# Performance work log

Hardware: AMD Instinct MI355X
Metric: run time of the kernel (lower is better)

## Reference

```python
import jax, jax.numpy as jnp
import numpy as np

NUM_HEADS = 12
EMB = 768
D_KEY = 64
D_VALUE = 64
MASKED = True


def setup_inputs() -> dict:
    key = jax.random.key(0)
    k1, k2, k3, k4 = jax.random.split(key, 4)
    x = jax.random.normal(k1, (1, 4096, EMB), dtype=jnp.float32)
    q_proj = jax.random.normal(k2, (NUM_HEADS, EMB, D_KEY), dtype=jnp.float32)
    k_proj = jax.random.normal(k3, (NUM_HEADS, EMB, D_KEY), dtype=jnp.float32)
    v_proj = jax.random.normal(k4, (NUM_HEADS, EMB, D_VALUE), dtype=jnp.float32)
    return {"x": x, "q_proj": q_proj, "k_proj": k_proj, "v_proj": v_proj}


def reference(x, q_proj, k_proj, v_proj):
    # x: [B, S, E]; projections: [H, E, dk/dv]
    q = jnp.einsum("bse,hek->bhsk", x, q_proj)  # [B,H,S,dk]
    k = jnp.einsum("bse,hek->bhsk", x, k_proj)  # [B,H,S,dk]
    v = jnp.einsum("bse,hev->bhsv", x, v_proj)  # [B,H,S,dv]
    scale = jnp.sqrt(jnp.asarray(D_KEY, dtype=x.dtype))
    scores = jnp.einsum("bhsk,bhtk->bhst", q, k) / scale  # [B,H,S,S]
    if MASKED:
        S = x.shape[1]
        # causal mask: disallow attending to future positions (strict upper triangle)
        mask = jnp.triu(jnp.ones((S, S), dtype=bool), k=1)
        scores = jnp.where(mask, -jnp.inf, scores)
    attn = jax.nn.softmax(scores, axis=-1)
    out = jnp.einsum("bhst,bhtv->bhsv", attn, v)  # [B,H,S,dv]
    return out
```

## Files before the change

kernel.cpp:

```cpp
#include <hip/hip_runtime.h>
#include <hip/hip_bf16.h>

#define NH 12
#define SEQ 4096
#define E 768
#define DK 64

typedef float f32x4 __attribute__((ext_vector_type(4)));
typedef float f32x16 __attribute__((ext_vector_type(16)));
typedef __bf16 bf16x8 __attribute__((ext_vector_type(8)));
typedef __bf16 bf16x4 __attribute__((ext_vector_type(4)));
typedef unsigned u32x2 __attribute__((ext_vector_type(2)));
typedef unsigned u32x4 __attribute__((ext_vector_type(4)));

#define MFMA16(a, b, c) __builtin_amdgcn_mfma_f32_16x16x32_bf16((a), (b), (c), 0, 0, 0)
#define MFMA32(a, b, c) __builtin_amdgcn_mfma_f32_32x32x16_bf16((a), (b), (c), 0, 0, 0)

#define SCL 0.18033688011112042f
#define DEFER 10.8f

__device__ __forceinline__ void gload16(const void* g, void* l) {
    __builtin_amdgcn_global_load_lds(
        (const __attribute__((address_space(1))) void*)g,
        (__attribute__((address_space(3))) void*)l, 16, 0, 0);
}

__device__ __forceinline__ void block_sync() {
    __builtin_amdgcn_sched_barrier(0);
    __builtin_amdgcn_s_barrier();
    __builtin_amdgcn_sched_barrier(0);
}

__device__ __forceinline__ unsigned cvtpk(float lo, float hi) {
    unsigned r;
    asm("v_cvt_pk_bf16_f32 %0, %1, %2" : "=v"(r) : "v"(lo), "v"(hi));
    return r;
}
__device__ __forceinline__ u32x2 plswap(unsigned a, unsigned b) {
    return __builtin_amdgcn_permlane32_swap(a, b, false, false);
}
__device__ __forceinline__ float xhalf_max(float v) {
    u32x2 r = plswap(__float_as_uint(v), __float_as_uint(v));
    return fmaxf(__uint_as_float(r.x), __uint_as_float(r.y));
}
__device__ __forceinline__ float xhalf_add(float v) {
    u32x2 r = plswap(__float_as_uint(v), __float_as_uint(v));
    return __uint_as_float(r.x) + __uint_as_float(r.y);
}

__global__ __launch_bounds__(256) void xsplit_kernel(const float* __restrict__ x,
                                                     __bf16* __restrict__ xh,
                                                     __bf16* __restrict__ xl) {
    int i = blockIdx.x * blockDim.x + threadIdx.x;
    float4 v = ((const float4*)x)[i];
    bf16x4 h, l;
    float vv[4] = {v.x, v.y, v.z, v.w};
#pragma unroll
    for (int j = 0; j < 4; ++j) {
        __bf16 hh = (__bf16)vv[j];
        h[j] = hh;
        l[j] = (__bf16)(vv[j] - (float)hh);
    }
    ((bf16x4*)xh)[i] = h;
    ((bf16x4*)xl)[i] = l;
}

__global__ void wsplit_kernel(const float* __restrict__ qp,
                              const float* __restrict__ kp,
                              const float* __restrict__ vp,
                              __bf16* __restrict__ wtq_h, __bf16* __restrict__ wtq_l,
                              __bf16* __restrict__ wtk_h, __bf16* __restrict__ wtk_l,
                              __bf16* __restrict__ wtv_h) {
    int idx = blockIdx.x * blockDim.x + threadIdx.x;
    if (idx >= NH * E * DK) return;
    int h = idx / (E * DK);
    int rem = idx - h * E * DK;
    int k = rem / DK;
    int n = rem - k * DK;
    int o = h * DK * E + n * E + k;
    float q = qp[idx];
    __bf16 qh = (__bf16)q;
    wtq_h[o] = qh;
    wtq_l[o] = (__bf16)(q - (float)qh);
    float kk = kp[idx] * SCL;
    __bf16 kh = (__bf16)kk;
    wtk_h[o] = kh;
    wtk_l[o] = (__bf16)(kk - (float)kh);
    wtv_h[o] = (__bf16)vp[idx];
}

__global__ __launch_bounds__(256, 2) void proj_qk_kernel(
    const __bf16* __restrict__ xh, const __bf16* __restrict__ xl,
    const __bf16* __restrict__ wq_h_g, const __bf16* __restrict__ wq_l_g,
    const __bf16* __restrict__ wk_h_g, const __bf16* __restrict__ wk_l_g,
    __bf16* __restrict__ qh_o, __bf16* __restrict__ ql_o,
    __bf16* __restrict__ kh_o, __bf16* __restrict__ kl_o) {
    __shared__ char wlds[2][16384];

    const int wg = (blockIdx.x & 7) * 96 + (blockIdx.x >> 3);
    const int head = wg >> 6;
    const int rb = wg & 63;
    const int wave = threadIdx.x >> 6;
    const int lane = threadIdx.x & 63;
    const int lrow = lane & 15;
    const int lk8 = (lane >> 4) * 8;
    const int g4 = (lane >> 4) * 4;
    const int rowbase = rb * 64 + wave * 16;

    const char* wq_h_b = (const char*)(wq_h_g + head * DK * E);
    const char* wq_l_b = (const char*)(wq_l_g + head * DK * E);
    const char* wk_h_b = (const char*)(wk_h_g + head * DK * E);
    const char* wk_l_b = (const char*)(wk_l_g + head * DK * E);
    const char* base = (wave == 0) ? wq_h_b : (wave == 1) ? wq_l_b
                      : (wave == 2) ? wk_h_b : wk_l_b;
    const int srow = lane >> 2;
    const int scol = (lane & 3) * 16;

    auto STAGE = [&](int buf, int ks) {
#pragma unroll
        for (int r = 0; r < 4; ++r) {
            const char* src = base + (size_t)(r * 16 + srow) * (E * 2) + ks * 64 + scol;
            gload16(src, wlds[buf] + (wave * 4 + r) * 1024 + lane * 16);
        }
    };

    f32x4 accq[4], acck[4];
#pragma unroll
    for (int f = 0; f < 4; ++f) {
        accq[f] = (f32x4){0.f, 0.f, 0.f, 0.f};
        acck[f] = (f32x4){0.f, 0.f, 0.f, 0.f};
    }

    bf16x8 ah, al, ahn, aln;
    auto LOADA = [&](int ks, bf16x8& h, bf16x8& l) {
        size_t xo = (size_t)(rowbase + lrow) * E + ks * 32 + lk8;
        h = *(const bf16x8*)(xh + xo);
        l = *(const bf16x8*)(xl + xo);
    };

    LOADA(0, ah, al);
    STAGE(0, 0);
    int buf = 0;
    for (int ks = 0; ks < 24; ++ks) {
        if (ks < 23) {
            LOADA(ks + 1, ahn, aln);
            STAGE(buf ^ 1, ks + 1);
            asm volatile("s_waitcnt vmcnt(6)" ::: "memory");
        } else {
            asm volatile("s_waitcnt vmcnt(0)" ::: "memory");
        }
        block_sync();
#pragma unroll
        for (int f = 0; f < 4; ++f) {
            int bo = (f * 16 + lrow) * 64 + lk8 * 2;
            bf16x8 bqh = *(const bf16x8*)(wlds[buf] + bo);
            bf16x8 bql = *(const bf16x8*)(wlds[buf] + 4096 + bo);
            bf16x8 bkh = *(const bf16x8*)(wlds[buf] + 8192 + bo);
            bf16x8 bkl = *(const bf16x8*)(wlds[buf] + 12288 + bo);
            accq[f] = MFMA16(ah, bqh, accq[f]);
            accq[f] = MFMA16(ah, bql, accq[f]);
            accq[f] = MFMA16(al, bqh, accq[f]);
            acck[f] = MFMA16(ah, bkh, acck[f]);
            acck[f] = MFMA16(ah, bkl, acck[f]);
            acck[f] = MFMA16(al, bkh, acck[f]);
        }
        block_sync();
        if (ks < 23) {
            ah = ahn;
            al = aln;
        }
        buf ^= 1;
    }

    char* khb = (char*)kh_o + (size_t)head * SEQ * DK * 2;
    char* klb = (char*)kl_o + (size_t)head * SEQ * DK * 2;
#pragma unroll
    for (int f = 0; f < 4; ++f)
#pragma unroll
        for (int r = 0; r < 4; ++r) {
            int srow_o = rowbase + g4 + r;
            int d = f * 16 + lrow;
            size_t o = (size_t)head * SEQ * DK + (size_t)srow_o * DK + d;
            float qv = accq[f][r];
            __bf16 qhh = (__bf16)qv;
            qh_o[o] = qhh;
            ql_o[o] = (__bf16)(qv - (float)qhh);
            size_t ko = (size_t)(srow_o >> 6) * 8192 + ((srow_o >> 5) & 1) * 4096
                      + (size_t)f * 1024
                      + ((srow_o & 31) + 32 * ((lrow >> 3) & 1)) * 16 + (lrow & 7) * 2;
            float kv = acck[f][r];
            __bf16 khh = (__bf16)kv;
            *(__bf16*)(khb + ko) = khh;
            *(__bf16*)(klb + ko) = (__bf16)(kv - (float)khh);
        }
}

__global__ __launch_bounds__(256) void proj_v_kernel(
    const __bf16* __restrict__ xh, const __bf16* __restrict__ w_v,
    __bf16* __restrict__ vt_o) {
    __shared__ char wlds[2][4096];

    const int wg = (blockIdx.x & 7) * 96 + (blockIdx.x >> 3);
    const int head = wg >> 6;
    const int rb = wg & 63;
    const int wave = threadIdx.x >> 6;
    const int lane = threadIdx.x & 63;
    const int lrow = lane & 15;
    const int lk8 = (lane >> 4) * 8;
    const int g4 = (lane >> 4) * 4;
    const int rowbase = rb * 64 + wave * 16;

    const char* wv_b = (const char*)(w_v + head * DK * E);
    const int srow = lane >> 2;
    const int scol = (lane & 3) * 16;

    auto STAGE = [&](int buf, int ks) {
        const char* src = wv_b + (size_t)(wave * 16 + srow) * (E * 2) + ks * 64 + scol;
        gload16(src, wlds[buf] + wave * 1024 + lane * 16);
    };

    f32x4 acc[4];
#pragma unroll
    for (int f = 0; f < 4; ++f) acc[f] = (f32x4){0.f, 0.f, 0.f, 0.f};

    bf16x8 ah, ahn;
    auto LOADA = [&](int ks, bf16x8& h) {
        size_t xo = (size_t)(rowbase + lrow) * E + ks * 32 + lk8;
        h = *(const bf16x8*)(xh + xo);
    };

    LOADA(0, ah);
    STAGE(0, 0);
    int buf = 0;
    for (int ks = 0; ks < 24; ++ks) {
        if (ks < 23) {
            LOADA(ks + 1, ahn);
            STAGE(buf ^ 1, ks + 1);
            asm volatile("s_waitcnt vmcnt(2)" ::: "memory");
        } else {
            asm volatile("s_waitcnt vmcnt(0)" ::: "memory");
        }
        block_sync();
#pragma unroll
        for (int f = 0; f < 4; ++f) {
            int bo = (f * 16 + lrow) * 64 + lk8 * 2;
            bf16x8 bv = *(const bf16x8*)(wlds[buf] + bo);
            acc[f] = MFMA16(bv, ah, acc[f]);
        }
        block_sync();
        if (ks < 23) ah = ahn;
        buf ^= 1;
    }

    char* vb = (char*)vt_o + (size_t)head * DK * SEQ * 2;
#pragma unroll
    for (int f = 0; f < 4; ++f)
#pragma unroll
        for (int r = 0; r < 4; ++r) {
            int vd = f * 16 + g4 + r;
            int vs = rowbase + lrow;
            size_t vo = (size_t)(vs >> 6) * 8192 + ((vd >> 5) & 1) * 4096
                      + ((vs >> 4) & 3) * 1024
                      + ((vd & 31) + 32 * ((vs >> 3) & 1)) * 16 + (vs & 7) * 2;
            *(__bf16*)(vb + vo) = (__bf16)acc[f][r];
        }
}

__global__ __launch_bounds__(256, 2) void attn_kernel(
    const __bf16* __restrict__ qh, const __bf16* __restrict__ ql,
    const __bf16* __restrict__ kh, const __bf16* __restrict__ kl,
    const __bf16* __restrict__ vt,
    float* __restrict__ out) {
    __shared__ float cbuf[3][64][33];
    __shared__ float mlb[4][2][32];

    const int wg = (blockIdx.x & 7) * 192 + (blockIdx.x >> 3);
    const int head = wg >> 7;
    const int window = 127 - (wg & 127);
    const int rowbase = window * 32;
    const int wave = threadIdx.x >> 6;
    const int lane = threadIdx.x & 63;
    const int lq = lane & 31;
    const int lh = lane >> 5;

    const size_t hoff = (size_t)head * SEQ * DK;

    bf16x8 qBh[4], qBl[4];
    {
        const __bf16* qph = qh + hoff + (size_t)(rowbase + lq) * DK + lh * 8;
        const __bf16* qpl = ql + hoff + (size_t)(rowbase + lq) * DK + lh * 8;
#pragma unroll
        for (int ds = 0; ds < 4; ++ds) {
            qBh[ds] = *(const bf16x8*)(qph + ds * 16);
            qBl[ds] = *(const bf16x8*)(qpl + ds * 16);
        }
    }

    const char* kh_p = (const char*)(kh + hoff) + wave * 8192 + lane * 16;
    const char* kl_p = (const char*)(kl + hoff) + wave * 8192 + lane * 16;
    const char* vt_p = (const char*)(vt + (size_t)head * DK * SEQ) + wave * 8192 + lane * 16;

    f32x16 O0 = (f32x16)0.0f, O1 = (f32x16)0.0f;
    float m = -3.0e38f, lsum = 0.f;

    const int nt = (window >> 1) + 1;

    for (int t = wave; t < nt; t += 4) {
        const int kb = t * 64;

        f32x16 s0 = (f32x16)0.0f, s1 = (f32x16)0.0f;
#pragma unroll
        for (int ds = 0; ds < 4; ++ds) {
            bf16x8 ah0 = *(const bf16x8*)(kh_p + ds * 1024);
            bf16x8 al0 = *(const bf16x8*)(kl_p + ds * 1024);
            bf16x8 ah1 = *(const bf16x8*)(kh_p + 4096 + ds * 1024);
            bf16x8 al1 = *(const bf16x8*)(kl_p + 4096 + ds * 1024);
            s0 = MFMA32(ah0, qBh[ds], s0);
            s1 = MFMA32(ah1, qBh[ds], s1);
            s0 = MFMA32(al0, qBh[ds], s0);
            s1 = MFMA32(al1, qBh[ds], s1);
            s0 = MFMA32(ah0, qBl[ds], s0);
            s1 = MFMA32(ah1, qBl[ds], s1);
        }

        bf16x8 v00 = *(const bf16x8*)(vt_p + 0);
        bf16x8 v01 = *(const bf16x8*)(vt_p + 1024);
        bf16x8 v10 = *(const bf16x8*)(vt_p + 2048);
        bf16x8 v11 = *(const bf16x8*)(vt_p + 3072);
        bf16x8 w00 = *(const bf16x8*)(vt_p + 4096);
        bf16x8 w01 = *(const bf16x8*)(vt_p + 5120);
        bf16x8 w10 = *(const bf16x8*)(vt_p + 6144);
        bf16x8 w11 = *(const bf16x8*)(vt_p + 7168);

        if (kb + 63 > rowbase) {
            int qa = rowbase + lq;
#pragma unroll
            for (int r = 0; r < 16; ++r) {
                int kp = kb + ((r & 3) + 8 * (r >> 2) + 4 * lh);
                if (kp > qa) s0[r] = -1.0e30f;
                if (kp + 32 > qa) s1[r] = -1.0e30f;
            }
        }

        float x0 = fmaxf(s0[0], s0[1]), x1 = fmaxf(s0[2], s0[3]);
        float x2 = fmaxf(s0[4], s0[5]), x3 = fmaxf(s0[6], s0[7]);
#pragma unroll
        for (int r = 8; r < 16; r += 4) {
            x0 = fmaxf(x0, fmaxf(s0[r], s0[r + 1]));
            x1 = fmaxf(x1, fmaxf(s0[r + 2], s0[r + 3]));
        }
#pragma unroll
        for (int r = 0; r < 16; r += 4) {
            x2 = fmaxf(x2, fmaxf(s1[r], s1[r + 1]));
            x3 = fmaxf(x3, fmaxf(s1[r + 2], s1[r + 3]));
        }
        float mx = xhalf_max(fmaxf(fmaxf(x0, x1), fmaxf(x2, x3)));

        if (!__all(mx - m <= DEFER)) {
            float mn = fmaxf(m, mx);
            float al = exp2f(m - mn);
            m = mn;
            lsum *= al;
#pragma unroll
            for (int r = 0; r < 16; ++r) {
                float a = __shfl(al, (r & 3) + 8 * (r >> 2) + 4 * lh);
                O0[r] *= a;
                O1[r] *= a;
            }
        }

        s0 = s0 - m;
        s1 = s1 - m;
#pragma unroll
        for (int r = 0; r < 16; ++r) {
            s0[r] = exp2f(s0[r]);
            s1[r] = exp2f(s1[r]);
        }
        {
            f32x16 sv = s0 + s1;
            float p0 = 0.f, p1 = 0.f;
#pragma unroll
            for (int r = 0; r < 16; r += 4) {
                p0 += sv[r] + sv[r + 1];
                p1 += sv[r + 2] + sv[r + 3];
            }
            lsum += p0 + p1;
        }

        unsigned W0 = cvtpk(s0[0], s0[1]), W1 = cvtpk(s0[2], s0[3]);
        unsigned W2 = cvtpk(s0[4], s0[5]), W3 = cvtpk(s0[6], s0[7]);
        unsigned W4 = cvtpk(s0[8], s0[9]), W5 = cvtpk(s0[10], s0[11]);
        unsigned W6 = cvtpk(s0[12], s0[13]), W7 = cvtpk(s0[14], s0[15]);
        u32x2 rA = plswap(W0, W2), rB = plswap(W1, W3);
        u32x2 rC = plswap(W4, W6), rD = plswap(W5, W7);
        bf16x8 p00 = __builtin_bit_cast(bf16x8, (u32x4){rA.x, rB.x, rA.y, rB.y});
        bf16x8 p01 = __builtin_bit_cast(bf16x8, (u32x4){rC.x, rD.x, rC.y, rD.y});
        W0 = cvtpk(s1[0], s1[1]); W1 = cvtpk(s1[2], s1[3]);
        W2 = cvtpk(s1[4], s1[5]); W3 = cvtpk(s1[6], s1[7]);
        W4 = cvtpk(s1[8], s1[9]); W5 = cvtpk(s1[10], s1[11]);
        W6 = cvtpk(s1[12], s1[13]); W7 = cvtpk(s1[14], s1[15]);
        rA = plswap(W0, W2); rB = plswap(W1, W3);
        rC = plswap(W4, W6); rD = plswap(W5, W7);
        bf16x8 p10 = __builtin_bit_cast(bf16x8, (u32x4){rA.x, rB.x, rA.y, rB.y});
        bf16x8 p11 = __builtin_bit_cast(bf16x8, (u32x4){rC.x, rD.x, rC.y, rD.y});

        O0 = MFMA32(p00, v00, O0);
        O0 = MFMA32(p01, v01, O0);
        O0 = MFMA32(p10, v10, O0);
        O0 = MFMA32(p11, v11, O0);
        O1 = MFMA32(p00, w00, O1);
        O1 = MFMA32(p01, w01, O1);
        O1 = MFMA32(p10, w10, O1);
        O1 = MFMA32(p11, w11, O1);

        kh_p += 4 * 8192;
        kl_p += 4 * 8192;
        vt_p += 4 * 8192;
    }

    if (lh == 0) mlb[wave][0][lq] = m;
    __syncthreads();
    float mstar = fmaxf(fmaxf(mlb[0][0][lq], mlb[1][0][lq]),
                        fmaxf(mlb[2][0][lq], mlb[3][0][lq]));
    float sc = exp2f(m - mstar);
    float lp = xhalf_add(lsum) * sc;
#pragma unroll
    for (int r = 0; r < 16; ++r) {
        float a = __shfl(sc, (r & 3) + 8 * (r >> 2) + 4 * lh);
        O0[r] *= a;
        O1[r] *= a;
    }
    if (wave > 0) {
        if (lh == 0) mlb[wave][1][lq] = lp;
        float* cb = &cbuf[wave - 1][lane][0];
#pragma unroll
        for (int r = 0; r < 16; ++r) {
            cb[r] = O0[r];
            cb[16 + r] = O1[r];
        }
    }
    __syncthreads();
    if (wave == 0) {
        float ltot = lp + mlb[1][1][lq] + mlb[2][1][lq] + mlb[3][1][lq];
#pragma unroll
        for (int i = 0; i < 3; ++i) {
            const float* cb = &cbuf[i][lane][0];
#pragma unroll
            for (int r = 0; r < 16; ++r) {
                O0[r] += cb[r];
                O1[r] += cb[16 + r];
            }
        }
        float linv = 1.0f / ltot;
#pragma unroll
        for (int r = 0; r < 16; ++r) {
            int rr = (r & 3) + 8 * (r >> 2) + 4 * lh;
            float li = __shfl(linv, rr);
            size_t o = hoff + (size_t)(rowbase + rr) * DK + lq;
            out[o] = O0[r] * li;
            out[o + 32] = O1[r] * li;
        }
    }
}

extern "C" void kernel_launch(void* const* d_in, const int* in_sizes, int n_in,
                              void* d_out, int out_size, void* d_ws, size_t ws_size,
                              hipStream_t stream) {
    const float* x = (const float*)d_in[0];
    const float* qp = (const float*)d_in[1];
    const float* kp = (const float*)d_in[2];
    const float* vp = (const float*)d_in[3];
    float* out = (float*)d_out;

    const size_t WT_SZ = (size_t)NH * DK * E * 2;
    const size_t QKV_SZ = (size_t)NH * SEQ * DK * 2;
    const size_t X_SZ = (size_t)SEQ * E * 2;
    char* ws = (char*)d_ws;
    __bf16* wtq_h = (__bf16*)(ws + 0 * WT_SZ);
    __bf16* wtq_l = (__bf16*)(ws + 1 * WT_SZ);
    __bf16* wtk_h = (__bf16*)(ws + 2 * WT_SZ);
    __bf16* wtk_l = (__bf16*)(ws + 3 * WT_SZ);
    __bf16* wtv_h = (__bf16*)(ws + 4 * WT_SZ);
    char* p2 = ws + 5 * WT_SZ;
    __bf16* qh = (__bf16*)(p2 + 0 * QKV_SZ);
    __bf16* ql = (__bf16*)(p2 + 1 * QKV_SZ);
    __bf16* kh = (__bf16*)(p2 + 2 * QKV_SZ);
    __bf16* kl = (__bf16*)(p2 + 3 * QKV_SZ);
    __bf16* vt = (__bf16*)(p2 + 4 * QKV_SZ);
    char* p3 = p2 + 5 * QKV_SZ;
    __bf16* xh = (__bf16*)(p3 + 0 * X_SZ);
    __bf16* xl = (__bf16*)(p3 + 1 * X_SZ);

    hipLaunchKernelGGL(xsplit_kernel, dim3(SEQ * E / 4 / 256), dim3(256), 0, stream,
                       x, xh, xl);
    hipLaunchKernelGGL(wsplit_kernel, dim3((NH * E * DK + 255) / 256), dim3(256), 0, stream,
                       qp, kp, vp, wtq_h, wtq_l, wtk_h, wtk_l, wtv_h);
    hipLaunchKernelGGL(proj_qk_kernel, dim3(768), dim3(256), 0, stream,
                       xh, xl, wtq_h, wtq_l, wtk_h, wtk_l, qh, ql, kh, kl);
    hipLaunchKernelGGL(proj_v_kernel, dim3(768), dim3(256), 0, stream,
                       xh, wtv_h, vt);
    hipLaunchKernelGGL(attn_kernel, dim3(1536), dim3(256), 0, stream,
                       qh, ql, kh, kl, vt, out);
}
```

Before: 176.9 us.

## Split causal attention into balanced per-wave KV tasks with separate combine kernel

Replaces the per-window workgroup, in which four waves stride over the KV tiles and combine through LDS, with a flat task list. Each wave now owns one (head, window, split) task, and later windows get more splits (1 to 4) to even out the causal triangle's work. Each task writes its bf16 partial O plus max and sum to the workspace, which overwrites the now-dead weight-split buffers. A second kernel merges the partials with log-sum-exp weighting. This trades an extra launch and global partial traffic, plus reduced precision in the partial O, for better load balance and no in-block barriers.

```diff
diff --git a/kernel.cpp b/kernel.cpp
--- a/kernel.cpp
+++ b/kernel.cpp
@@ -18,6 +18,10 @@
 
 #define SCL 0.18033688011112042f
 #define DEFER 10.8f
+
+#define TPH 320
+#define NTASK 3840
+#define PART_SZ 4352
 
 __device__ __forceinline__ void gload16(const void* g, void* l) {
     __builtin_amdgcn_global_load_lds(
@@ -266,22 +270,29 @@
         }
 }
 
-__global__ __launch_bounds__(256, 2) void attn_kernel(
+__global__ __launch_bounds__(256, 2) void attn_part_kernel(
     const __bf16* __restrict__ qh, const __bf16* __restrict__ ql,
     const __bf16* __restrict__ kh, const __bf16* __restrict__ kl,
     const __bf16* __restrict__ vt,
-    float* __restrict__ out) {
-    __shared__ float cbuf[3][64][33];
-    __shared__ float mlb[4][2][32];
-
-    const int wg = (blockIdx.x & 7) * 192 + (blockIdx.x >> 3);
-    const int head = wg >> 7;
-    const int window = 127 - (wg & 127);
-    const int rowbase = window * 32;
+    char* __restrict__ part) {
+    const int blk = (blockIdx.x & 7) * 120 + (blockIdx.x >> 3);
     const int wave = threadIdx.x >> 6;
+    const int task = blk * 4 + wave;
     const int lane = threadIdx.x & 63;
     const int lq = lane & 31;
     const int lh = lane >> 5;
+
+    const int head = task / TPH;
+    const int t = task - head * TPH;
+    int w, split, nsp;
+    if (t < 32)       { w = t;                             split = 0;     nsp = 1; }
+    else if (t < 96)  { int u = t - 32;  w = 32 + (u >> 1); split = u & 1; nsp = 2; }
+    else if (t < 192) { int u = t - 96;  w = 64 + u / 3;    split = u % 3; nsp = 3; }
+    else              { int u = t - 192; w = 96 + (u >> 2); split = u & 3; nsp = 4; }
+    const int ktot = (w >> 1) + 1;
+    const int lo = (split * ktot) / nsp;
+    const int hi = ((split + 1) * ktot) / nsp;
+    const int rowbase = w * 32;
 
     const size_t hoff = (size_t)head * SEQ * DK;
 
@@ -296,17 +307,15 @@
         }
     }
 
-    const char* kh_p = (const char*)(kh + hoff) + wave * 8192 + lane * 16;
-    const char* kl_p = (const char*)(kl + hoff) + wave * 8192 + lane * 16;
-    const char* vt_p = (const char*)(vt + (size_t)head * DK * SEQ) + wave * 8192 + lane * 16;
+    const char* kh_p = (const char*)(kh + hoff) + (size_t)lo * 8192 + lane * 16;
+    const char* kl_p = (const char*)(kl + hoff) + (size_t)lo * 8192 + lane * 16;
+    const char* vt_p = (const char*)(vt + (size_t)head * DK * SEQ) + (size_t)lo * 8192 + lane * 16;
 
     f32x16 O0 = (f32x16)0.0f, O1 = (f32x16)0.0f;
     float m = -3.0e38f, lsum = 0.f;
 
-    const int nt = (window >> 1) + 1;
-
-    for (int t = wave; t < nt; t += 4) {
-        const int kb = t * 64;
+    for (int tt = lo; tt < hi; ++tt) {
+        const int kb = tt * 64;
 
         f32x16 s0 = (f32x16)0.0f, s1 = (f32x16)0.0f;
 #pragma unroll
@@ -413,54 +422,74 @@
         O1 = MFMA32(p10, w10, O1);
         O1 = MFMA32(p11, w11, O1);
 
-        kh_p += 4 * 8192;
-        kl_p += 4 * 8192;
-        vt_p += 4 * 8192;
-    }
-
-    if (lh == 0) mlb[wave][0][lq] = m;
-    __syncthreads();
-    float mstar = fmaxf(fmaxf(mlb[0][0][lq], mlb[1][0][lq]),
-                        fmaxf(mlb[2][0][lq], mlb[3][0][lq]));
-    float sc = exp2f(m - mstar);
-    float lp = xhalf_add(lsum) * sc;
-#pragma unroll
-    for (int r = 0; r < 16; ++r) {
-        float a = __shfl(sc, (r & 3) + 8 * (r >> 2) + 4 * lh);
-        O0[r] *= a;
-        O1[r] *= a;
-    }
-    if (wave > 0) {
-        if (lh == 0) mlb[wave][1][lq] = lp;
-        float* cb = &cbuf[wave - 1][lane][0];
-#pragma unroll
-        for (int r = 0; r < 16; ++r) {
-            cb[r] = O0[r];
-            cb[16 + r] = O1[r];
-        }
-    }
-    __syncthreads();
-    if (wave == 0) {
-        float ltot = lp + mlb[1][1][lq] + mlb[2][1][lq] + mlb[3][1][lq];
-#pragma unroll
-        for (int i = 0; i < 3; ++i) {
-            const float* cb = &cbuf[i][lane][0];
-#pragma unroll
-            for (int r = 0; r < 16; ++r) {
-                O0[r] += cb[r];
-                O1[r] += cb[16 + r];
-            }
-        }
-        float linv = 1.0f / ltot;
-#pragma unroll
-        for (int r = 0; r < 16; ++r) {
-            int rr = (r & 3) + 8 * (r >> 2) + 4 * lh;
-            float li = __shfl(linv, rr);
-            size_t o = hoff + (size_t)(rowbase + rr) * DK + lq;
-            out[o] = O0[r] * li;
-            out[o + 32] = O1[r] * li;
-        }
-    }
+        kh_p += 8192;
+        kl_p += 8192;
+        vt_p += 8192;
+    }
+
+    char* pb = part + (size_t)task * PART_SZ;
+    unsigned* ph = (unsigned*)pb;
+#pragma unroll
+    for (int r = 0; r < 16; r += 2) {
+        ph[(r >> 1) * 64 + lane] = cvtpk(O0[r], O0[r + 1]);
+        ph[512 + (r >> 1) * 64 + lane] = cvtpk(O1[r], O1[r + 1]);
+    }
+    float lf = xhalf_add(lsum);
+    float* pm = (float*)(pb + 4096);
+    if (lane < 32) {
+        pm[lq] = m;
+        pm[32 + lq] = lf;
+    }
+}
+
+__global__ __launch_bounds__(256) void attn_comb_kernel(
+    const char* __restrict__ part, float* __restrict__ out) {
+    const int W = blockIdx.x;
+    const int head = W >> 7, w = W & 127;
+    int tb, nsp;
+    if (w < 32)      { tb = w;                 nsp = 1; }
+    else if (w < 64) { tb = 32 + (w - 32) * 2; nsp = 2; }
+    else if (w < 96) { tb = 96 + (w - 64) * 3; nsp = 3; }
+    else             { tb = 192 + (w - 96) * 4; nsp = 4; }
+    tb += head * TPH;
+
+    const int tid = threadIdx.x;
+    const int row = tid >> 3;
+    const int d0 = (tid & 7) * 8;
+    const int lane0 = (d0 & 31) + 32 * ((row >> 2) & 1);
+    const int r = (row & 3) + 4 * (row >> 3);
+    const int word = (r >> 1) * 64;
+    const int hi16 = r & 1;
+    const char* p0 = part + (size_t)tb * PART_SZ;
+
+    float mv[4], lv[4];
+    float mstar = -3.0e38f;
+    for (int s = 0; s < nsp; ++s) {
+        const float* pm = (const float*)(p0 + s * PART_SZ + 4096);
+        mv[s] = pm[row];
+        lv[s] = pm[32 + row];
+        mstar = fmaxf(mstar, mv[s]);
+    }
+
+    float acc[8] = {0.f, 0.f, 0.f, 0.f, 0.f, 0.f, 0.f, 0.f};
+    float lt = 0.f;
+    for (int s = 0; s < nsp; ++s) {
+        float wgt = exp2f(mv[s] - mstar);
+        lt += wgt * lv[s];
+        const unsigned* pw = (const unsigned*)(p0 + s * PART_SZ + (d0 >> 5) * 2048);
+        u32x4 a = *(const u32x4*)(pw + word + lane0);
+        u32x4 b = *(const u32x4*)(pw + word + lane0 + 4);
+#pragma unroll
+        for (int j = 0; j < 8; ++j) {
+            unsigned u = (j < 4) ? a[j] : b[j - 4];
+            unsigned bits = hi16 ? (u & 0xffff0000u) : (u << 16);
+            acc[j] += wgt * __uint_as_float(bits);
+        }
+    }
+    float inv = 1.0f / lt;
+    size_t o = (size_t)head * SEQ * DK + (size_t)(w * 32 + row) * DK + d0;
+#pragma unroll
+    for (int j = 0; j < 8; ++j) out[o + j] = acc[j] * inv;
 }
 
 extern "C" void kernel_launch(void* const* d_in, const int* in_sizes, int n_in,
@@ -481,15 +510,16 @@
     __bf16* wtk_h = (__bf16*)(ws + 2 * WT_SZ);
     __bf16* wtk_l = (__bf16*)(ws + 3 * WT_SZ);
     __bf16* wtv_h = (__bf16*)(ws + 4 * WT_SZ);
-    char* p2 = ws + 5 * WT_SZ;
+    char* px = ws + 5 * WT_SZ;
+    __bf16* xh = (__bf16*)(px + 0 * X_SZ);
+    __bf16* xl = (__bf16*)(px + 1 * X_SZ);
+    char* p2 = px + 2 * X_SZ;
     __bf16* qh = (__bf16*)(p2 + 0 * QKV_SZ);
     __bf16* ql = (__bf16*)(p2 + 1 * QKV_SZ);
     __bf16* kh = (__bf16*)(p2 + 2 * QKV_SZ);
     __bf16* kl = (__bf16*)(p2 + 3 * QKV_SZ);
     __bf16* vt = (__bf16*)(p2 + 4 * QKV_SZ);
-    char* p3 = p2 + 5 * QKV_SZ;
-    __bf16* xh = (__bf16*)(p3 + 0 * X_SZ);
-    __bf16* xl = (__bf16*)(p3 + 1 * X_SZ);
+    char* part = ws;
 
     hipLaunchKernelGGL(xsplit_kernel, dim3(SEQ * E / 4 / 256), dim3(256), 0, stream,
                        x, xh, xl);
@@ -499,6 +529,8 @@
                        xh, xl, wtq_h, wtq_l, wtk_h, wtk_l, qh, ql, kh, kl);
     hipLaunchKernelGGL(proj_v_kernel, dim3(768), dim3(256), 0, stream,
                        xh, wtv_h, vt);
-    hipLaunchKernelGGL(attn_kernel, dim3(1536), dim3(256), 0, stream,
-                       qh, ql, kh, kl, vt, out);
-}
+    hipLaunchKernelGGL(attn_part_kernel, dim3(960), dim3(256), 0, stream,
+                       qh, ql, kh, kl, vt, part);
+    hipLaunchKernelGGL(attn_comb_kernel, dim3(1536), dim3(256), 0, stream,
+                       part, out);
+}
```

Result: slower. 187.8 us (+6.2%).

## Fuse V projection into QK projection and process two query blocks per attention workgroup

Applied to the files above, without the earlier changes.

The V projection kernel is merged into the QK projection kernel. One extra weight tile is staged per k-step and the x tile already in registers is reused, so one launch and a second pass over x are removed. The attention kernel now has each workgroup handle two adjacent 32-row query blocks (64 rows) against each K/V tile, halving K/V loads per query row and the grid size. The costs are higher register pressure and larger LDS use, possible lower occupancy, and coarser load balance across the causal triangle.

```diff
diff --git a/kernel.cpp b/kernel.cpp
--- a/kernel.cpp
+++ b/kernel.cpp
@@ -89,13 +89,15 @@
     wtv_h[o] = (__bf16)vp[idx];
 }
 
-__global__ __launch_bounds__(256, 2) void proj_qk_kernel(
+__global__ __launch_bounds__(256, 2) void proj_kernel(
     const __bf16* __restrict__ xh, const __bf16* __restrict__ xl,
     const __bf16* __restrict__ wq_h_g, const __bf16* __restrict__ wq_l_g,
     const __bf16* __restrict__ wk_h_g, const __bf16* __restrict__ wk_l_g,
+    const __bf16* __restrict__ wv_g,
     __bf16* __restrict__ qh_o, __bf16* __restrict__ ql_o,
-    __bf16* __restrict__ kh_o, __bf16* __restrict__ kl_o) {
-    __shared__ char wlds[2][16384];
+    __bf16* __restrict__ kh_o, __bf16* __restrict__ kl_o,
+    __bf16* __restrict__ vt_o) {
+    __shared__ char wlds[2][20480];
 
     const int wg = (blockIdx.x & 7) * 96 + (blockIdx.x >> 3);
     const int head = wg >> 6;
@@ -107,28 +109,28 @@
     const int g4 = (lane >> 4) * 4;
     const int rowbase = rb * 64 + wave * 16;
 
-    const char* wq_h_b = (const char*)(wq_h_g + head * DK * E);
-    const char* wq_l_b = (const char*)(wq_l_g + head * DK * E);
-    const char* wk_h_b = (const char*)(wk_h_g + head * DK * E);
-    const char* wk_l_b = (const char*)(wk_l_g + head * DK * E);
-    const char* base = (wave == 0) ? wq_h_b : (wave == 1) ? wq_l_b
-                      : (wave == 2) ? wk_h_b : wk_l_b;
+    const char* bases[5] = {
+        (const char*)(wq_h_g + head * DK * E), (const char*)(wq_l_g + head * DK * E),
+        (const char*)(wk_h_g + head * DK * E), (const char*)(wk_l_g + head * DK * E),
+        (const char*)(wv_g + head * DK * E)};
     const int srow = lane >> 2;
     const int scol = (lane & 3) * 16;
 
     auto STAGE = [&](int buf, int ks) {
 #pragma unroll
-        for (int r = 0; r < 4; ++r) {
-            const char* src = base + (size_t)(r * 16 + srow) * (E * 2) + ks * 64 + scol;
-            gload16(src, wlds[buf] + (wave * 4 + r) * 1024 + lane * 16);
+        for (int r = 0; r < 5; ++r) {
+            int q = wave * 5 + r;
+            const char* src = bases[q >> 2] + (size_t)((q & 3) * 16 + srow) * (E * 2) + ks * 64 + scol;
+            gload16(src, wlds[buf] + q * 1024 + lane * 16);
         }
     };
 
-    f32x4 accq[4], acck[4];
+    f32x4 accq[4], acck[4], accv[4];
 #pragma unroll
     for (int f = 0; f < 4; ++f) {
         accq[f] = (f32x4){0.f, 0.f, 0.f, 0.f};
         acck[f] = (f32x4){0.f, 0.f, 0.f, 0.f};
+        accv[f] = (f32x4){0.f, 0.f, 0.f, 0.f};
     }
 
     bf16x8 ah, al, ahn, aln;
@@ -145,7 +147,7 @@
         if (ks < 23) {
             LOADA(ks + 1, ahn, aln);
             STAGE(buf ^ 1, ks + 1);
-            asm volatile("s_waitcnt vmcnt(6)" ::: "memory");
+            asm volatile("s_waitcnt vmcnt(7)" ::: "memory");
         } else {
             asm volatile("s_waitcnt vmcnt(0)" ::: "memory");
         }
@@ -157,12 +159,14 @@
             bf16x8 bql = *(const bf16x8*)(wlds[buf] + 4096 + bo);
             bf16x8 bkh = *(const bf16x8*)(wlds[buf] + 8192 + bo);
             bf16x8 bkl = *(const bf16x8*)(wlds[buf] + 12288 + bo);
+            bf16x8 bv  = *(const bf16x8*)(wlds[buf] + 16384 + bo);
             accq[f] = MFMA16(ah, bqh, accq[f]);
             accq[f] = MFMA16(ah, bql, accq[f]);
             accq[f] = MFMA16(al, bqh, accq[f]);
             acck[f] = MFMA16(ah, bkh, acck[f]);
             acck[f] = MFMA16(ah, bkl, acck[f]);
             acck[f] = MFMA16(al, bkh, acck[f]);
+            accv[f] = MFMA16(bv, ah, accv[f]);
         }
         block_sync();
         if (ks < 23) {
@@ -174,6 +178,7 @@
 
     char* khb = (char*)kh_o + (size_t)head * SEQ * DK * 2;
     char* klb = (char*)kl_o + (size_t)head * SEQ * DK * 2;
+    char* vb = (char*)vt_o + (size_t)head * DK * SEQ * 2;
 #pragma unroll
     for (int f = 0; f < 4; ++f)
 #pragma unroll
@@ -192,77 +197,12 @@
             __bf16 khh = (__bf16)kv;
             *(__bf16*)(khb + ko) = khh;
             *(__bf16*)(klb + ko) = (__bf16)(kv - (float)khh);
-        }
-}
-
-__global__ __launch_bounds__(256) void proj_v_kernel(
-    const __bf16* __restrict__ xh, const __bf16* __restrict__ w_v,
-    __bf16* __restrict__ vt_o) {
-    __shared__ char wlds[2][4096];
-
-    const int wg = (blockIdx.x & 7) * 96 + (blockIdx.x >> 3);
-    const int head = wg >> 6;
-    const int rb = wg & 63;
-    const int wave = threadIdx.x >> 6;
-    const int lane = threadIdx.x & 63;
-    const int lrow = lane & 15;
-    const int lk8 = (lane >> 4) * 8;
-    const int g4 = (lane >> 4) * 4;
-    const int rowbase = rb * 64 + wave * 16;
-
-    const char* wv_b = (const char*)(w_v + head * DK * E);
-    const int srow = lane >> 2;
-    const int scol = (lane & 3) * 16;
-
-    auto STAGE = [&](int buf, int ks) {
-        const char* src = wv_b + (size_t)(wave * 16 + srow) * (E * 2) + ks * 64 + scol;
-        gload16(src, wlds[buf] + wave * 1024 + lane * 16);
-    };
-
-    f32x4 acc[4];
-#pragma unroll
-    for (int f = 0; f < 4; ++f) acc[f] = (f32x4){0.f, 0.f, 0.f, 0.f};
-
-    bf16x8 ah, ahn;
-    auto LOADA = [&](int ks, bf16x8& h) {
-        size_t xo = (size_t)(rowbase + lrow) * E + ks * 32 + lk8;
-        h = *(const bf16x8*)(xh + xo);
-    };
-
-    LOADA(0, ah);
-    STAGE(0, 0);
-    int buf = 0;
-    for (int ks = 0; ks < 24; ++ks) {
-        if (ks < 23) {
-            LOADA(ks + 1, ahn);
-            STAGE(buf ^ 1, ks + 1);
-            asm volatile("s_waitcnt vmcnt(2)" ::: "memory");
-        } else {
-            asm volatile("s_waitcnt vmcnt(0)" ::: "memory");
-        }
-        block_sync();
-#pragma unroll
-        for (int f = 0; f < 4; ++f) {
-            int bo = (f * 16 + lrow) * 64 + lk8 * 2;
-            bf16x8 bv = *(const bf16x8*)(wlds[buf] + bo);
-            acc[f] = MFMA16(bv, ah, acc[f]);
-        }
-        block_sync();
-        if (ks < 23) ah = ahn;
-        buf ^= 1;
-    }
-
-    char* vb = (char*)vt_o + (size_t)head * DK * SEQ * 2;
-#pragma unroll
-    for (int f = 0; f < 4; ++f)
-#pragma unroll
-        for (int r = 0; r < 4; ++r) {
             int vd = f * 16 + g4 + r;
             int vs = rowbase + lrow;
             size_t vo = (size_t)(vs >> 6) * 8192 + ((vd >> 5) & 1) * 4096
                       + ((vs >> 4) & 3) * 1024
                       + ((vd & 31) + 32 * ((vs >> 3) & 1)) * 16 + (vs & 7) * 2;
-            *(__bf16*)(vb + vo) = (__bf16)acc[f][r];
+            *(__bf16*)(vb + vo) = (__bf16)accv[f][r];
         }
 }
 
@@ -271,13 +211,15 @@
     const __bf16* __restrict__ kh, const __bf16* __restrict__ kl,
     const __bf16* __restrict__ vt,
     float* __restrict__ out) {
-    __shared__ float cbuf[3][64][33];
-    __shared__ float mlb[4][2][32];
-
-    const int wg = (blockIdx.x & 7) * 192 + (blockIdx.x >> 3);
-    const int head = wg >> 7;
-    const int window = 127 - (wg & 127);
-    const int rowbase = window * 32;
+    __shared__ float cbuf[2][3][64][33];
+    __shared__ float mlb[4][2][2][32];
+
+    const int wg = (blockIdx.x & 7) * 96 + (blockIdx.x >> 3);
+    const int head = wg >> 6;
+    const int pr = 63 - (wg & 63);
+    const int rowb0 = pr * 64;
+    const int rowb1 = pr * 64 + 32;
+    const int nt = pr + 1;
     const int wave = threadIdx.x >> 6;
     const int lane = threadIdx.x & 63;
     const int lq = lane & 31;
@@ -285,63 +227,32 @@
 
     const size_t hoff = (size_t)head * SEQ * DK;
 
-    bf16x8 qBh[4], qBl[4];
+    bf16x8 qAh[4], qAl[4], qBh[4], qBl[4];
     {
-        const __bf16* qph = qh + hoff + (size_t)(rowbase + lq) * DK + lh * 8;
-        const __bf16* qpl = ql + hoff + (size_t)(rowbase + lq) * DK + lh * 8;
+        const __bf16* pA = qh + hoff + (size_t)(rowb0 + lq) * DK + lh * 8;
+        const __bf16* lA = ql + hoff + (size_t)(rowb0 + lq) * DK + lh * 8;
+        const __bf16* pB = qh + hoff + (size_t)(rowb1 + lq) * DK + lh * 8;
+        const __bf16* lB = ql + hoff + (size_t)(rowb1 + lq) * DK + lh * 8;
 #pragma unroll
         for (int ds = 0; ds < 4; ++ds) {
-            qBh[ds] = *(const bf16x8*)(qph + ds * 16);
-            qBl[ds] = *(const bf16x8*)(qpl + ds * 16);
-        }
-    }
-
-    const char* kh_p = (const char*)(kh + hoff) + wave * 8192 + lane * 16;
-    const char* kl_p = (const char*)(kl + hoff) + wave * 8192 + lane * 16;
-    const char* vt_p = (const char*)(vt + (size_t)head * DK * SEQ) + wave * 8192 + lane * 16;
-
-    f32x16 O0 = (f32x16)0.0f, O1 = (f32x16)0.0f;
-    float m = -3.0e38f, lsum = 0.f;
-
-    const int nt = (window >> 1) + 1;
-
-    for (int t = wave; t < nt; t += 4) {
-        const int kb = t * 64;
-
-        f32x16 s0 = (f32x16)0.0f, s1 = (f32x16)0.0f;
-#pragma unroll
-        for (int ds = 0; ds < 4; ++ds) {
-            bf16x8 ah0 = *(const bf16x8*)(kh_p + ds * 1024);
-            bf16x8 al0 = *(const bf16x8*)(kl_p + ds * 1024);
-            bf16x8 ah1 = *(const bf16x8*)(kh_p + 4096 + ds * 1024);
-            bf16x8 al1 = *(const bf16x8*)(kl_p + 4096 + ds * 1024);
-            s0 = MFMA32(ah0, qBh[ds], s0);
-            s1 = MFMA32(ah1, qBh[ds], s1);
-            s0 = MFMA32(al0, qBh[ds], s0);
-            s1 = MFMA32(al1, qBh[ds], s1);
-            s0 = MFMA32(ah0, qBl[ds], s0);
-            s1 = MFMA32(ah1, qBl[ds], s1);
-        }
-
-        bf16x8 v00 = *(const bf16x8*)(vt_p + 0);
-        bf16x8 v01 = *(const bf16x8*)(vt_p + 1024);
-        bf16x8 v10 = *(const bf16x8*)(vt_p + 2048);
-        bf16x8 v11 = *(const bf16x8*)(vt_p + 3072);
-        bf16x8 w00 = *(const bf16x8*)(vt_p + 4096);
-        bf16x8 w01 = *(const bf16x8*)(vt_p + 5120);
-        bf16x8 w10 = *(const bf16x8*)(vt_p + 6144);
-        bf16x8 w11 = *(const bf16x8*)(vt_p + 7168);
-
-        if (kb + 63 > rowbase) {
-            int qa = rowbase + lq;
-#pragma unroll
-            for (int r = 0; r < 16; ++r) {
-                int kp = kb + ((r & 3) + 8 * (r >> 2) + 4 * lh);
-                if (kp > qa) s0[r] = -1.0e30f;
-                if (kp + 32 > qa) s1[r] = -1.0e30f;
-            }
-        }
-
+            qAh[ds] = *(const bf16x8*)(pA + ds * 16);
+            qAl[ds] = *(const bf16x8*)(lA + ds * 16);
+            qBh[ds] = *(const bf16x8*)(pB + ds * 16);
+            qBl[ds] = *(const bf16x8*)(lB + ds * 16);
+        }
+    }
+
+    const char* kh_p = (const char*)(kh + hoff) + (size_t)wave * 8192 + lane * 16;
+    const char* kl_p = (const char*)(kl + hoff) + (size_t)wave * 8192 + lane * 16;
+    const char* vt_p = (const char*)(vt + (size_t)head * DK * SEQ) + (size_t)wave * 8192 + lane * 16;
+
+    f32x16 OA0 = (f32x16)0.0f, OA1 = (f32x16)0.0f;
+    f32x16 OB0 = (f32x16)0.0f, OB1 = (f32x16)0.0f;
+    float mA = -3.0e38f, lsA = 0.f, mB = -3.0e38f, lsB = 0.f;
+
+    auto SOFTMAX = [&](f32x16& s0, f32x16& s1, float& m, float& ls,
+                       f32x16& O0, f32x16& O1,
+                       bf16x8& p00, bf16x8& p01, bf16x8& p10, bf16x8& p11) {
         float x0 = fmaxf(s0[0], s0[1]), x1 = fmaxf(s0[2], s0[3]);
         float x2 = fmaxf(s0[4], s0[5]), x3 = fmaxf(s0[6], s0[7]);
 #pragma unroll
@@ -355,12 +266,11 @@
             x3 = fmaxf(x3, fmaxf(s1[r + 2], s1[r + 3]));
         }
         float mx = xhalf_max(fmaxf(fmaxf(x0, x1), fmaxf(x2, x3)));
-
         if (!__all(mx - m <= DEFER)) {
             float mn = fmaxf(m, mx);
             float al = exp2f(m - mn);
             m = mn;
-            lsum *= al;
+            ls *= al;
 #pragma unroll
             for (int r = 0; r < 16; ++r) {
                 float a = __shfl(al, (r & 3) + 8 * (r >> 2) + 4 * lh);
@@ -368,7 +278,6 @@
                 O1[r] *= a;
             }
         }
-
         s0 = s0 - m;
         s1 = s1 - m;
 #pragma unroll
@@ -384,81 +293,164 @@
                 p0 += sv[r] + sv[r + 1];
                 p1 += sv[r + 2] + sv[r + 3];
             }
-            lsum += p0 + p1;
-        }
-
+            ls += p0 + p1;
+        }
         unsigned W0 = cvtpk(s0[0], s0[1]), W1 = cvtpk(s0[2], s0[3]);
         unsigned W2 = cvtpk(s0[4], s0[5]), W3 = cvtpk(s0[6], s0[7]);
         unsigned W4 = cvtpk(s0[8], s0[9]), W5 = cvtpk(s0[10], s0[11]);
         unsigned W6 = cvtpk(s0[12], s0[13]), W7 = cvtpk(s0[14], s0[15]);
         u32x2 rA = plswap(W0, W2), rB = plswap(W1, W3);
         u32x2 rC = plswap(W4, W6), rD = plswap(W5, W7);
-        bf16x8 p00 = __builtin_bit_cast(bf16x8, (u32x4){rA.x, rB.x, rA.y, rB.y});
-        bf16x8 p01 = __builtin_bit_cast(bf16x8, (u32x4){rC.x, rD.x, rC.y, rD.y});
+        p00 = __builtin_bit_cast(bf16x8, (u32x4){rA.x, rB.x, rA.y, rB.y});
+        p01 = __builtin_bit_cast(bf16x8, (u32x4){rC.x, rD.x, rC.y, rD.y});
         W0 = cvtpk(s1[0], s1[1]); W1 = cvtpk(s1[2], s1[3]);
         W2 = cvtpk(s1[4], s1[5]); W3 = cvtpk(s1[6], s1[7]);
         W4 = cvtpk(s1[8], s1[9]); W5 = cvtpk(s1[10], s1[11]);
         W6 = cvtpk(s1[12], s1[13]); W7 = cvtpk(s1[14], s1[15]);
         rA = plswap(W0, W2); rB = plswap(W1, W3);
         rC = plswap(W4, W6); rD = plswap(W5, W7);
-        bf16x8 p10 = __builtin_bit_cast(bf16x8, (u32x4){rA.x, rB.x, rA.y, rB.y});
-        bf16x8 p11 = __builtin_bit_cast(bf16x8, (u32x4){rC.x, rD.x, rC.y, rD.y});
-
-        O0 = MFMA32(p00, v00, O0);
-        O0 = MFMA32(p01, v01, O0);
-        O0 = MFMA32(p10, v10, O0);
-        O0 = MFMA32(p11, v11, O0);
-        O1 = MFMA32(p00, w00, O1);
-        O1 = MFMA32(p01, w01, O1);
-        O1 = MFMA32(p10, w10, O1);
-        O1 = MFMA32(p11, w11, O1);
+        p10 = __builtin_bit_cast(bf16x8, (u32x4){rA.x, rB.x, rA.y, rB.y});
+        p11 = __builtin_bit_cast(bf16x8, (u32x4){rC.x, rD.x, rC.y, rD.y});
+    };
+
+    for (int t = wave; t < nt; t += 4) {
+        const int kb = t * 64;
+
+        f32x16 sA0 = (f32x16)0.0f, sA1 = (f32x16)0.0f;
+        f32x16 sB0 = (f32x16)0.0f, sB1 = (f32x16)0.0f;
+#pragma unroll
+        for (int ds = 0; ds < 4; ++ds) {
+            bf16x8 ah0 = *(const bf16x8*)(kh_p + ds * 1024);
+            bf16x8 al0 = *(const bf16x8*)(kl_p + ds * 1024);
+            bf16x8 ah1 = *(const bf16x8*)(kh_p + 4096 + ds * 1024);
+            bf16x8 al1 = *(const bf16x8*)(kl_p + 4096 + ds * 1024);
+            sA0 = MFMA32(ah0, qAh[ds], sA0);
+            sA1 = MFMA32(ah1, qAh[ds], sA1);
+            sB0 = MFMA32(ah0, qBh[ds], sB0);
+            sB1 = MFMA32(ah1, qBh[ds], sB1);
+            sA0 = MFMA32(al0, qAh[ds], sA0);
+            sA1 = MFMA32(al1, qAh[ds], sA1);
+            sB0 = MFMA32(al0, qBh[ds], sB0);
+            sB1 = MFMA32(al1, qBh[ds], sB1);
+            sA0 = MFMA32(ah0, qAl[ds], sA0);
+            sA1 = MFMA32(ah1, qAl[ds], sA1);
+            sB0 = MFMA32(ah0, qBl[ds], sB0);
+            sB1 = MFMA32(ah1, qBl[ds], sB1);
+        }
+
+        if (t == nt - 1) {
+            int qa0 = rowb0 + lq, qa1 = rowb1 + lq;
+#pragma unroll
+            for (int r = 0; r < 16; ++r) {
+                int kp = kb + ((r & 3) + 8 * (r >> 2) + 4 * lh);
+                if (kp > qa0) sA0[r] = -1.0e30f;
+                if (kp + 32 > qa0) sA1[r] = -1.0e30f;
+                if (kp > qa1) sB0[r] = -1.0e30f;
+                if (kp + 32 > qa1) sB1[r] = -1.0e30f;
+            }
+        }
+
+        bf16x8 pA00, pA01, pA10, pA11, pB00, pB01, pB10, pB11;
+        SOFTMAX(sA0, sA1, mA, lsA, OA0, OA1, pA00, pA01, pA10, pA11);
+        SOFTMAX(sB0, sB1, mB, lsB, OB0, OB1, pB00, pB01, pB10, pB11);
+
+        {
+            bf16x8 v00 = *(const bf16x8*)(vt_p + 0);
+            bf16x8 v01 = *(const bf16x8*)(vt_p + 1024);
+            bf16x8 v10 = *(const bf16x8*)(vt_p + 2048);
+            bf16x8 v11 = *(const bf16x8*)(vt_p + 3072);
+            OA0 = MFMA32(pA00, v00, OA0);
+            OB0 = MFMA32(pB00, v00, OB0);
+            OA0 = MFMA32(pA01, v01, OA0);
+            OB0 = MFMA32(pB01, v01, OB0);
+            OA0 = MFMA32(pA10, v10, OA0);
+            OB0 = MFMA32(pB10, v10, OB0);
+            OA0 = MFMA32(pA11, v11, OA0);
+            OB0 = MFMA32(pB11, v11, OB0);
+            bf16x8 w00 = *(const bf16x8*)(vt_p + 4096);
+            bf16x8 w01 = *(const bf16x8*)(vt_p + 5120);
+            bf16x8 w10 = *(const bf16x8*)(vt_p + 6144);
+            bf16x8 w11 = *(const bf16x8*)(vt_p + 7168);
+            OA1 = MFMA32(pA00, w00, OA1);
+            OB1 = MFMA32(pB00, w00, OB1);
+            OA1 = MFMA32(pA01, w01, OA1);
+            OB1 = MFMA32(pB01, w01, OB1);
+            OA1 = MFMA32(pA10, w10, OA1);
+            OB1 = MFMA32(pB10, w10, OB1);
+            OA1 = MFMA32(pA11, w11, OA1);
+            OB1 = MFMA32(pB11, w11, OB1);
+        }
 
         kh_p += 4 * 8192;
         kl_p += 4 * 8192;
         vt_p += 4 * 8192;
     }
 
-    if (lh == 0) mlb[wave][0][lq] = m;
+    if (lh == 0) {
+        mlb[wave][0][0][lq] = mA;
+        mlb[wave][1][0][lq] = mB;
+    }
     __syncthreads();
-    float mstar = fmaxf(fmaxf(mlb[0][0][lq], mlb[1][0][lq]),
-                        fmaxf(mlb[2][0][lq], mlb[3][0][lq]));
-    float sc = exp2f(m - mstar);
-    float lp = xhalf_add(lsum) * sc;
+    float msA = fmaxf(fmaxf(mlb[0][0][0][lq], mlb[1][0][0][lq]),
+                      fmaxf(mlb[2][0][0][lq], mlb[3][0][0][lq]));
+    float msB = fmaxf(fmaxf(mlb[0][1][0][lq], mlb[1][1][0][lq]),
+                      fmaxf(mlb[2][1][0][lq], mlb[3][1][0][lq]));
+    float scA = exp2f(mA - msA), scB = exp2f(mB - msB);
+    float lpA = xhalf_add(lsA) * scA;
+    float lpB = xhalf_add(lsB) * scB;
 #pragma unroll
     for (int r = 0; r < 16; ++r) {
-        float a = __shfl(sc, (r & 3) + 8 * (r >> 2) + 4 * lh);
-        O0[r] *= a;
-        O1[r] *= a;
+        int rr = (r & 3) + 8 * (r >> 2) + 4 * lh;
+        float a = __shfl(scA, rr);
+        float b = __shfl(scB, rr);
+        OA0[r] *= a;
+        OA1[r] *= a;
+        OB0[r] *= b;
+        OB1[r] *= b;
     }
     if (wave > 0) {
-        if (lh == 0) mlb[wave][1][lq] = lp;
-        float* cb = &cbuf[wave - 1][lane][0];
+        if (lh == 0) {
+            mlb[wave][0][1][lq] = lpA;
+            mlb[wave][1][1][lq] = lpB;
+        }
+        float* ca = &cbuf[0][wave - 1][lane][0];
+        float* cb = &cbuf[1][wave - 1][lane][0];
 #pragma unroll
         for (int r = 0; r < 16; ++r) {
-            cb[r] = O0[r];
-            cb[16 + r] = O1[r];
+            ca[r] = OA0[r];
+            ca[16 + r] = OA1[r];
+            cb[r] = OB0[r];
+            cb[16 + r] = OB1[r];
         }
     }
     __syncthreads();
     if (wave == 0) {
-        float ltot = lp + mlb[1][1][lq] + mlb[2][1][lq] + mlb[3][1][lq];
+        float ltA = lpA + mlb[1][0][1][lq] + mlb[2][0][1][lq] + mlb[3][0][1][lq];
+        float ltB = lpB + mlb[1][1][1][lq] + mlb[2][1][1][lq] + mlb[3][1][1][lq];
 #pragma unroll
         for (int i = 0; i < 3; ++i) {
-            const float* cb = &cbuf[i][lane][0];
+            const float* ca = &cbuf[0][i][lane][0];
+            const float* cb = &cbuf[1][i][lane][0];
 #pragma unroll
             for (int r = 0; r < 16; ++r) {
-                O0[r] += cb[r];
-                O1[r] += cb[16 + r];
+                OA0[r] += ca[r];
+                OA1[r] += ca[16 + r];
+                OB0[r] += cb[r];
+                OB1[r] += cb[16 + r];
             }
         }
-        float linv = 1.0f / ltot;
+        float invA = 1.0f / ltA, invB = 1.0f / ltB;
 #pragma unroll
         for (int r = 0; r < 16; ++r) {
             int rr = (r & 3) + 8 * (r >> 2) + 4 * lh;
-            float li = __shfl(linv, rr);
-            size_t o = hoff + (size_t)(rowbase + rr) * DK + lq;
-            out[o] = O0[r] * li;
-            out[o + 32] = O1[r] * li;
+            float la = __shfl(invA, rr);
+            float lb = __shfl(invB, rr);
+            size_t oa = hoff + (size_t)(rowb0 + rr) * DK + lq;
+            size_t ob = hoff + (size_t)(rowb1 + rr) * DK + lq;
+            out[oa] = OA0[r] * la;
+            out[oa + 32] = OA1[r] * la;
+            out[ob] = OB0[r] * lb;
+            out[ob + 32] = OB1[r] * lb;
         }
     }
 }
@@ -481,24 +473,22 @@
     __bf16* wtk_h = (__bf16*)(ws + 2 * WT_SZ);
     __bf16* wtk_l = (__bf16*)(ws + 3 * WT_SZ);
     __bf16* wtv_h = (__bf16*)(ws + 4 * WT_SZ);
-    char* p2 = ws + 5 * WT_SZ;
+    char* px = ws + 5 * WT_SZ;
+    __bf16* xh = (__bf16*)(px + 0 * X_SZ);
+    __bf16* xl = (__bf16*)(px + 1 * X_SZ);
+    char* p2 = px + 2 * X_SZ;
     __bf16* qh = (__bf16*)(p2 + 0 * QKV_SZ);
     __bf16* ql = (__bf16*)(p2 + 1 * QKV_SZ);
     __bf16* kh = (__bf16*)(p2 + 2 * QKV_SZ);
     __bf16* kl = (__bf16*)(p2 + 3 * QKV_SZ);
     __bf16* vt = (__bf16*)(p2 + 4 * QKV_SZ);
-    char* p3 = p2 + 5 * QKV_SZ;
-    __bf16* xh = (__bf16*)(p3 + 0 * X_SZ);
-    __bf16* xl = (__bf16*)(p3 + 1 * X_SZ);
 
     hipLaunchKernelGGL(xsplit_kernel, dim3(SEQ * E / 4 / 256), dim3(256), 0, stream,
                        x, xh, xl);
     hipLaunchKernelGGL(wsplit_kernel, dim3((NH * E * DK + 255) / 256), dim3(256), 0, stream,
                        qp, kp, vp, wtq_h, wtq_l, wtk_h, wtk_l, wtv_h);
-    hipLaunchKernelGGL(proj_qk_kernel, dim3(768), dim3(256), 0, stream,
-                       xh, xl, wtq_h, wtq_l, wtk_h, wtk_l, qh, ql, kh, kl);
-    hipLaunchKernelGGL(proj_v_kernel, dim3(768), dim3(256), 0, stream,
-                       xh, wtv_h, vt);
-    hipLaunchKernelGGL(attn_kernel, dim3(1536), dim3(256), 0, stream,
+    hipLaunchKernelGGL(proj_kernel, dim3(768), dim3(256), 0, stream,
+                       xh, xl, wtq_h, wtq_l, wtk_h, wtk_l, wtv_h, qh, ql, kh, kl, vt);
+    hipLaunchKernelGGL(attn_kernel, dim3(768), dim3(256), 0, stream,
                        qh, ql, kh, kl, vt, out);
 }
```

Result: slower. 197.1 us (+11.4%).
